# Performance work log

Hardware: AMD Instinct MI355X
Metric: run time of the kernel (lower is better)

## Reference

```python
import jax, jax.numpy as jnp
import numpy as np

N_NODES = 100_000
N_EDGES = 1_600_000
DIM = 64


def setup_inputs() -> dict:
    key = jax.random.key(0)
    ks = jax.random.split(key, 5)
    x = jax.random.normal(ks[0], (N_NODES, DIM), dtype=jnp.float32)
    edge_index = jax.random.randint(ks[1], (2, N_EDGES), 0, N_NODES, dtype=jnp.int64)
    scale = 1.0 / np.sqrt(DIM)
    W1 = jax.random.normal(ks[2], (DIM, DIM), dtype=jnp.float32) * scale
    b1 = jnp.zeros((DIM,), dtype=jnp.float32)
    W2 = jax.random.normal(ks[3], (DIM, DIM), dtype=jnp.float32) * scale
    b2 = jnp.zeros((DIM,), dtype=jnp.float32)
    return {"x": x, "edge_index": edge_index, "W1": W1, "b1": b1, "W2": W2, "b2": b2}


def reference(x, edge_index, W1, b1, W2, b2):
    # PyG GINEConv with edge_attr=None: message = relu(x_j) gathered over src edges
    src, dst = edge_index[0], edge_index[1]
    msg = jax.nn.relu(x[src])                                   # [E, dim] gather + relu
    agg = jax.ops.segment_sum(msg, dst, num_segments=x.shape[0])  # [N, dim] scatter-sum
    h = (1.0 + 0.0) * x + agg                                   # eps = 0 (train_eps=False)
    # gin_nn: Linear -> ReLU -> Linear
    h = jax.nn.relu(h @ W1 + b1) @ W2 + b2
    # outer F.relu; dropout is identity in eval mode
    return jax.nn.relu(h)
```

## Files before the change

kernel.cpp:

```cpp
#include <hip/hip_runtime.h>

#define N_NODES 100000
#define N_EDGES 1600000
#define DIM 64

#define BIN_SHIFT 9
#define BIN_NODES 512
#define NBINS ((N_NODES + BIN_NODES - 1) / BIN_NODES)
#define CAP 10240

#define TILE_A 8192
#define NBLK_A ((N_EDGES + TILE_A - 1) / TILE_A)
#define EPT (TILE_A / 512)

#define SCAT_BLOCKS  NBLK_A
#define PREP_BLOCKS  (N_NODES * DIM / 4 / 512)
#define WPREP_BLOCKS 16

typedef __attribute__((ext_vector_type(8))) short bf16x8;
typedef __attribute__((ext_vector_type(4))) float f32x4;

__device__ __forceinline__ float bflo(unsigned u) { return __uint_as_float(u << 16); }
__device__ __forceinline__ float bfhi(unsigned u) { return __uint_as_float(u & 0xFFFF0000u); }
__device__ __forceinline__ unsigned f2bf(float f) {
    unsigned u = __float_as_uint(f);
    u += 0x7FFFu + ((u >> 16) & 1u);
    return u >> 16;
}

__global__ __launch_bounds__(512) void prep_scatter(
    const float* __restrict__ x, unsigned* __restrict__ rx,
    const float* __restrict__ W1, const float* __restrict__ W2,
    unsigned short* __restrict__ Wpk,
    const int* __restrict__ ei,
    unsigned* __restrict__ binned,
    int* __restrict__ tblc, int* __restrict__ tblb)
{
    __shared__ int lhist[NBINS];
    __shared__ int lbase[NBINS];
    __shared__ int lcur[NBINS];
    __shared__ int ls[512];
    __shared__ unsigned staged[TILE_A];

    const int t   = threadIdx.x;
    const int blk = blockIdx.x;

    if (blk < SCAT_BLOCKS) {
        const int e0 = blk * TILE_A;
        const int n  = min(TILE_A, N_EDGES - e0);

        for (int i = t; i < NBINS; i += 512) { lhist[i] = 0; lcur[i] = 0; }
        __syncthreads();

        int      mybin[EPT];
        unsigned myval[EPT];
        #pragma unroll
        for (int q = 0; q < EPT / 4; ++q) {
            const int idx4 = q * 2048 + t * 4;
            if (idx4 < n) {
                const int4 s4 = *reinterpret_cast<const int4*>(ei + e0 + idx4);
                const int4 d4 = *reinterpret_cast<const int4*>(ei + N_EDGES + e0 + idx4);
                const int ss[4] = {s4.x, s4.y, s4.z, s4.w};
                const int dd[4] = {d4.x, d4.y, d4.z, d4.w};
                #pragma unroll
                for (int j = 0; j < 4; ++j) {
                    mybin[q * 4 + j] = dd[j] >> BIN_SHIFT;
                    myval[q * 4 + j] = ((unsigned)ss[j] << BIN_SHIFT)
                                     | (unsigned)(dd[j] & (BIN_NODES - 1));
                    atomicAdd(&lhist[dd[j] >> BIN_SHIFT], 1);
                }
            } else {
                #pragma unroll
                for (int j = 0; j < 4; ++j) mybin[q * 4 + j] = -1;
            }
        }
        __syncthreads();

        ls[t] = (t < NBINS) ? lhist[t] : 0;
        __syncthreads();
        #pragma unroll
        for (int d = 1; d < 512; d <<= 1) {
            const int add = (t >= d) ? ls[t - d] : 0;
            __syncthreads();
            ls[t] += add;
            __syncthreads();
        }
        if (t < NBINS) lbase[t] = ls[t] - lhist[t];
        __syncthreads();

        for (int i = t; i < NBINS; i += 512) {
            tblc[blk * NBINS + i] = lhist[i];
            tblb[blk * NBINS + i] = lbase[i];
        }

        #pragma unroll
        for (int j = 0; j < EPT; ++j) {
            if (mybin[j] >= 0) {
                const int p = lbase[mybin[j]] + atomicAdd(&lcur[mybin[j]], 1);
                staged[p] = myval[j];
            }
        }
        __syncthreads();

        for (int p = t; p < n; p += 512)
            binned[e0 + p] = staged[p];

    } else if (blk < SCAT_BLOCKS + PREP_BLOCKS) {
        const int i = (blk - SCAT_BLOCKS) * 512 + t;
        const float4 v = reinterpret_cast<const float4*>(x)[i];
        uint2 o;
        o.x = f2bf(fmaxf(v.x, 0.f)) | (f2bf(fmaxf(v.y, 0.f)) << 16);
        o.y = f2bf(fmaxf(v.z, 0.f)) | (f2bf(fmaxf(v.w, 0.f)) << 16);
        reinterpret_cast<uint2*>(rx)[i] = o;

    } else {
        const int idx = (blk - SCAT_BLOCKS - PREP_BLOCKS) * 512 + t;
        if (idx >= 8192) return;
        const int j    = idx & 7;
        const int lane = (idx >> 3) & 63;
        const int kk   = (idx >> 9) & 1;
        const int n    = (idx >> 10) & 3;
        const int L    = idx >> 12;
        const float* W = L ? W2 : W1;
        const int k    = kk * 32 + (lane >> 4) * 8 + j;
        const int col  = n * 16 + (lane & 15);
        Wpk[idx] = (unsigned short)f2bf(W[k * DIM + col]);
    }
}

__global__ __launch_bounds__(256) void binsort(
    const unsigned* __restrict__ binned,
    const int* __restrict__ tblc, const int* __restrict__ tblb,
    int* __restrict__ start,
    int* __restrict__ dega,
    int* __restrict__ slot)
{
    __shared__ int lhist[BIN_NODES];
    __shared__ int lofs[BIN_NODES];
    __shared__ int lcur[BIN_NODES];
    __shared__ int ls[256];
    __shared__ int sseg[CAP];

    const int b     = blockIdx.x;
    const int node0 = b << BIN_SHIFT;
    const int nloc  = min(BIN_NODES, N_NODES - node0);
    const int rbase = b * CAP;
    const int t     = threadIdx.x;

    for (int i = t; i < BIN_NODES; i += 256) { lhist[i] = 0; lcur[i] = 0; }
    __syncthreads();

    for (int sb = t; sb < NBLK_A; sb += 256) {
        const int cnt  = tblc[sb * NBINS + b];
        const int base = sb * TILE_A + tblb[sb * NBINS + b];
        for (int i = 0; i < cnt; ++i)
            atomicAdd(&lhist[binned[base + i] & (BIN_NODES - 1)], 1);
    }
    __syncthreads();

    const int a0 = lhist[2 * t];
    const int a1 = lhist[2 * t + 1];
    const int ps = a0 + a1;
    ls[t] = ps;
    __syncthreads();
    #pragma unroll
    for (int d = 1; d < 256; d <<= 1) {
        const int add = (t >= d) ? ls[t - d] : 0;
        __syncthreads();
        ls[t] += add;
        __syncthreads();
    }
    const int pbase = ls[t] - ps;
    lofs[2 * t]     = pbase;
    lofs[2 * t + 1] = pbase + a0;
    __syncthreads();

    const int total = min(lofs[BIN_NODES - 1] + lhist[BIN_NODES - 1], CAP);

    for (int i = t; i < nloc; i += 256) {
        start[node0 + i] = rbase + lofs[i];
        dega[node0 + i]  = lhist[i];
    }

    for (int sb = t; sb < NBLK_A; sb += 256) {
        const int cnt  = tblc[sb * NBINS + b];
        const int base = sb * TILE_A + tblb[sb * NBINS + b];
        for (int i = 0; i < cnt; ++i) {
            const unsigned v = binned[base + i];
            const int dl  = v & (BIN_NODES - 1);
            const int rel = lofs[dl] + atomicAdd(&lcur[dl], 1);
            if (rel < CAP) sseg[rel] = (int)(v >> BIN_SHIFT);
        }
    }
    __syncthreads();

    for (int p = t; p < total; p += 256)
        slot[rbase + p] = sseg[p];
}

__global__ __launch_bounds__(256) void gather_mlp(
    const float* __restrict__ x,
    const unsigned char* __restrict__ rx,
    const int*   __restrict__ start,
    const int*   __restrict__ dega,
    const int*   __restrict__ slot,
    const unsigned short* __restrict__ Wpk,
    const float* __restrict__ b1,
    const float* __restrict__ b2,
    float* __restrict__ out)
{
    __shared__ unsigned ht[32 * 36];
    __shared__ float yt[2][16 * 68];

    const int t    = threadIdx.x;
    const int wv   = t >> 6;
    const int lane = t & 63;
    const int g    = lane >> 3;
    const int c    = lane & 7;
    const int row  = wv * 8 + g;
    const int node = blockIdx.x * 32 + row;

    {
        const int beg = start[node];
        const int end = beg + dega[node];

        float acc[8];
        #pragma unroll
        for (int e = 0; e < 8; ++e) acc[e] = 0.f;

        for (int kb = beg; kb < end; kb += 8) {
            const int sv = (kb + c < end) ? slot[kb + c] : 0;

            int srcs[8];
            #pragma unroll
            for (int j = 0; j < 8; ++j) {
                const int s = __shfl(sv, g * 8 + j, 64);
                srcs[j] = (kb + j < end) ? s : 0;
            }
            uint4 buf[8];
            #pragma unroll
            for (int j = 0; j < 8; ++j)
                buf[j] = *reinterpret_cast<const uint4*>(
                    rx + (size_t)srcs[j] * 128 + c * 16);
            #pragma unroll
            for (int j = 0; j < 8; ++j) {
                if (kb + j < end) {
                    acc[0] += bflo(buf[j].x); acc[1] += bfhi(buf[j].x);
                    acc[2] += bflo(buf[j].y); acc[3] += bfhi(buf[j].y);
                    acc[4] += bflo(buf[j].z); acc[5] += bfhi(buf[j].z);
                    acc[6] += bflo(buf[j].w); acc[7] += bfhi(buf[j].w);
                }
            }
        }

        const float4 x0 = *reinterpret_cast<const float4*>(
            x + (size_t)node * DIM + c * 8);
        const float4 x1 = *reinterpret_cast<const float4*>(
            x + (size_t)node * DIM + c * 8 + 4);
        uint4 o;
        o.x = f2bf(x0.x + acc[0]) | (f2bf(x0.y + acc[1]) << 16);
        o.y = f2bf(x0.z + acc[2]) | (f2bf(x0.w + acc[3]) << 16);
        o.z = f2bf(x1.x + acc[4]) | (f2bf(x1.y + acc[5]) << 16);
        o.w = f2bf(x1.z + acc[6]) | (f2bf(x1.w + acc[7]) << 16);
        *reinterpret_cast<uint4*>(&ht[row * 36 + c * 4]) = o;
    }
    __syncthreads();

    if (wv >= 2) return;

    const int lrow = lane & 15;
    const int lgrp = lane >> 4;
    const int row2 = wv * 16 + lrow;

    union UF { uint4 u; bf16x8 v; };
    UF ha0, ha1;
    ha0.u = *reinterpret_cast<const uint4*>(&ht[row2 * 36 + lgrp * 4]);
    ha1.u = *reinterpret_cast<const uint4*>(&ht[row2 * 36 + 16 + lgrp * 4]);

    const uint4* wp = reinterpret_cast<const uint4*>(Wpk);

    float* my = &yt[wv][0];
    #pragma unroll
    for (int n = 0; n < 4; ++n) {
        const float bi = b1[n * 16 + lrow];
        f32x4 acc = {bi, bi, bi, bi};
        UF bw0, bw1;
        bw0.u = wp[(n * 2 + 0) * 64 + lane];
        bw1.u = wp[(n * 2 + 1) * 64 + lane];
        acc = __builtin_amdgcn_mfma_f32_16x16x32_bf16(ha0.v, bw0.v, acc, 0, 0, 0);
        acc = __builtin_amdgcn_mfma_f32_16x16x32_bf16(ha1.v, bw1.v, acc, 0, 0, 0);
        #pragma unroll
        for (int i = 0; i < 4; ++i)
            my[(lgrp * 4 + i) * 68 + n * 16 + lrow] = fmaxf(acc[i], 0.f);
    }

    const float* yr = &yt[wv][lrow * 68 + lgrp * 8];
    const float4 p0 = *reinterpret_cast<const float4*>(yr + 0);
    const float4 p1 = *reinterpret_cast<const float4*>(yr + 4);
    const float4 p2 = *reinterpret_cast<const float4*>(yr + 32);
    const float4 p3 = *reinterpret_cast<const float4*>(yr + 36);

    union UB { bf16x8 v; unsigned short s[8]; };
    UB ya0, ya1;
    ya0.s[0] = (unsigned short)f2bf(p0.x); ya0.s[1] = (unsigned short)f2bf(p0.y);
    ya0.s[2] = (unsigned short)f2bf(p0.z); ya0.s[3] = (unsigned short)f2bf(p0.w);
    ya0.s[4] = (unsigned short)f2bf(p1.x); ya0.s[5] = (unsigned short)f2bf(p1.y);
    ya0.s[6] = (unsigned short)f2bf(p1.z); ya0.s[7] = (unsigned short)f2bf(p1.w);
    ya1.s[0] = (unsigned short)f2bf(p2.x); ya1.s[1] = (unsigned short)f2bf(p2.y);
    ya1.s[2] = (unsigned short)f2bf(p2.z); ya1.s[3] = (unsigned short)f2bf(p2.w);
    ya1.s[4] = (unsigned short)f2bf(p3.x); ya1.s[5] = (unsigned short)f2bf(p3.y);
    ya1.s[6] = (unsigned short)f2bf(p3.z); ya1.s[7] = (unsigned short)f2bf(p3.w);

    #pragma unroll
    for (int n = 0; n < 4; ++n) {
        const float bi = b2[n * 16 + lrow];
        f32x4 acc = {bi, bi, bi, bi};
        UF bw0, bw1;
        bw0.u = wp[(8 + n * 2 + 0) * 64 + lane];
        bw1.u = wp[(8 + n * 2 + 1) * 64 + lane];
        acc = __builtin_amdgcn_mfma_f32_16x16x32_bf16(ya0.v, bw0.v, acc, 0, 0, 0);
        acc = __builtin_amdgcn_mfma_f32_16x16x32_bf16(ya1.v, bw1.v, acc, 0, 0, 0);
        const int r = blockIdx.x * 32 + wv * 16 + lgrp * 4;
        #pragma unroll
        for (int i = 0; i < 4; ++i)
            out[(size_t)(r + i) * DIM + n * 16 + lrow] = fmaxf(acc[i], 0.f);
    }
}

extern "C" void kernel_launch(void* const* d_in, const int* in_sizes, int n_in,
                              void* d_out, int out_size, void* d_ws, size_t ws_size,
                              hipStream_t stream) {
    const float* x  = (const float*)d_in[0];
    const int*   ei = (const int*)d_in[1];
    const float* W1 = (const float*)d_in[2];
    const float* b1 = (const float*)d_in[3];
    const float* W2 = (const float*)d_in[4];
    const float* b2 = (const float*)d_in[5];
    float* out = (float*)d_out;

    int* start = (int*)d_ws;
    int* dega  = start + 100352;
    int* tblc  = dega + 100352;
    int* tblb  = tblc + 40960;
    int* slot  = tblb + 40960;
    unsigned* binned = (unsigned*)(slot + NBINS * CAP);
    unsigned* rx     = binned + NBLK_A * TILE_A;
    unsigned short* Wpk =
        (unsigned short*)(rx + (size_t)N_NODES * 32);

    prep_scatter<<<SCAT_BLOCKS + PREP_BLOCKS + WPREP_BLOCKS, 512, 0, stream>>>(
        x, rx, W1, W2, Wpk, ei, binned, tblc, tblb);

    binsort<<<NBINS, 256, 0, stream>>>(binned, tblc, tblb, start, dega, slot);

    gather_mlp<<<3125, 256, 0, stream>>>(
        x, (const unsigned char*)rx, start, dega, slot, Wpk, b1, b2, out);
}
```

Measured before the change: 72.05 us.

## Stage bin edges into LDS once in binsort with flattened parallel load

```diff
diff --git a/kernel.cpp b/kernel.cpp
--- a/kernel.cpp
+++ b/kernel.cpp
@@ -128,18 +128,21 @@
     }
 }
 
-__global__ __launch_bounds__(256) void binsort(
+__global__ __launch_bounds__(512) void binsort(
     const unsigned* __restrict__ binned,
     const int* __restrict__ tblc, const int* __restrict__ tblb,
     int* __restrict__ start,
     int* __restrict__ dega,
     int* __restrict__ slot)
 {
+    __shared__ unsigned staged[CAP];
+    __shared__ int sseg[CAP];
     __shared__ int lhist[BIN_NODES];
     __shared__ int lofs[BIN_NODES];
     __shared__ int lcur[BIN_NODES];
-    __shared__ int ls[256];
-    __shared__ int sseg[CAP];
+    __shared__ int ls[512];
+    __shared__ int r_ofs[NBLK_A + 1];
+    __shared__ int r_base[NBLK_A];
 
     const int b     = blockIdx.x;
     const int node0 = b << BIN_SHIFT;
@@ -147,54 +150,66 @@
     const int rbase = b * CAP;
     const int t     = threadIdx.x;
 
-    for (int i = t; i < BIN_NODES; i += 256) { lhist[i] = 0; lcur[i] = 0; }
-    __syncthreads();
-
-    for (int sb = t; sb < NBLK_A; sb += 256) {
-        const int cnt  = tblc[sb * NBINS + b];
-        const int base = sb * TILE_A + tblb[sb * NBINS + b];
-        for (int i = 0; i < cnt; ++i)
-            atomicAdd(&lhist[binned[base + i] & (BIN_NODES - 1)], 1);
-    }
-    __syncthreads();
-
-    const int a0 = lhist[2 * t];
-    const int a1 = lhist[2 * t + 1];
-    const int ps = a0 + a1;
-    ls[t] = ps;
+    const int rc = (t < NBLK_A) ? tblc[t * NBINS + b] : 0;
+    if (t < NBLK_A) r_base[t] = t * TILE_A + tblb[t * NBINS + b];
+    ls[t] = rc;
     __syncthreads();
     #pragma unroll
-    for (int d = 1; d < 256; d <<= 1) {
+    for (int d = 1; d < 512; d <<= 1) {
         const int add = (t >= d) ? ls[t - d] : 0;
         __syncthreads();
         ls[t] += add;
         __syncthreads();
     }
-    const int pbase = ls[t] - ps;
-    lofs[2 * t]     = pbase;
-    lofs[2 * t + 1] = pbase + a0;
-    __syncthreads();
-
-    const int total = min(lofs[BIN_NODES - 1] + lhist[BIN_NODES - 1], CAP);
-
-    for (int i = t; i < nloc; i += 256) {
-        start[node0 + i] = rbase + lofs[i];
-        dega[node0 + i]  = lhist[i];
-    }
-
-    for (int sb = t; sb < NBLK_A; sb += 256) {
-        const int cnt  = tblc[sb * NBINS + b];
-        const int base = sb * TILE_A + tblb[sb * NBINS + b];
-        for (int i = 0; i < cnt; ++i) {
-            const unsigned v = binned[base + i];
-            const int dl  = v & (BIN_NODES - 1);
-            const int rel = lofs[dl] + atomicAdd(&lcur[dl], 1);
-            if (rel < CAP) sseg[rel] = (int)(v >> BIN_SHIFT);
-        }
-    }
-    __syncthreads();
-
-    for (int p = t; p < total; p += 256)
+    if (t < NBLK_A) r_ofs[t] = ls[t] - rc;
+    if (t == NBLK_A - 1) r_ofs[NBLK_A] = ls[t];
+    for (int i = t; i < BIN_NODES; i += 512) { lhist[i] = 0; lcur[i] = 0; }
+    __syncthreads();
+
+    const int cnt = min(r_ofs[NBLK_A], CAP);
+
+    for (int p = t; p < cnt; p += 512) {
+        int lo = 0, hi = NBLK_A - 1;
+        #pragma unroll
+        for (int s = 0; s < 8; ++s) {
+            const int mid = (lo + hi + 1) >> 1;
+            if (r_ofs[mid] <= p) lo = mid; else hi = mid - 1;
+        }
+        staged[p] = binned[r_base[lo] + (p - r_ofs[lo])];
+    }
+    __syncthreads();
+
+    for (int p = t; p < cnt; p += 512)
+        atomicAdd(&lhist[staged[p] & (BIN_NODES - 1)], 1);
+    __syncthreads();
+
+    const int v = lhist[t];
+    ls[t] = v;
+    __syncthreads();
+    #pragma unroll
+    for (int d = 1; d < 512; d <<= 1) {
+        const int add = (t >= d) ? ls[t - d] : 0;
+        __syncthreads();
+        ls[t] += add;
+        __syncthreads();
+    }
+    lofs[t] = ls[t] - v;
+    __syncthreads();
+
+    if (t < nloc) {
+        start[node0 + t] = rbase + lofs[t];
+        dega[node0 + t]  = lhist[t];
+    }
+
+    for (int p = t; p < cnt; p += 512) {
+        const unsigned e = staged[p];
+        const int dl  = e & (BIN_NODES - 1);
+        const int rel = lofs[dl] + atomicAdd(&lcur[dl], 1);
+        sseg[rel] = (int)(e >> BIN_SHIFT);
+    }
+    __syncthreads();
+
+    for (int p = t; p < cnt; p += 512)
         slot[rbase + p] = sseg[p];
 }
 
@@ -351,7 +366,7 @@
     prep_scatter<<<SCAT_BLOCKS + PREP_BLOCKS + WPREP_BLOCKS, 512, 0, stream>>>(
         x, rx, W1, W2, Wpk, ei, binned, tblc, tblb);
 
-    binsort<<<NBINS, 256, 0, stream>>>(binned, tblc, tblb, start, dega, slot);
+    binsort<<<NBINS, 512, 0, stream>>>(binned, tblc, tblb, start, dega, slot);
 
     gather_mlp<<<3125, 256, 0, stream>>>(
         x, (const unsigned char*)rx, start, dega, slot, Wpk, b1, b2, out);
```

Measured after the change: 66.61 us. -7.6%, faster.
